# Performance work log

Hardware: AMD Instinct MI355X
Metric: run time of the kernel (lower is better)

Reference implementation:

```python
import jax, jax.numpy as jnp
import numpy as np

L, B, T, H = 4, 64, 256, 1024  # layers, batch, seq_len, hidden (=input=output size)


def setup_inputs() -> dict:
    key = jax.random.key(0)
    ks = jax.random.split(key, 5)
    s = 0.03  # ~1/sqrt(H) init scale to avoid gate saturation
    return {
        "x": jax.random.normal(ks[0], (B, T, H), dtype=jnp.float32),
        "W_ih": jax.random.normal(ks[1], (L, 4 * H, H), dtype=jnp.float32) * s,
        "W_hh": jax.random.normal(ks[2], (L, 4 * H, H), dtype=jnp.float32) * s,
        "b_ih": jax.random.normal(ks[3], (L, 4 * H), dtype=jnp.float32) * s,
        "b_hh": jax.random.normal(ks[4], (L, 4 * H), dtype=jnp.float32) * s,
    }


def _lstm_cell(xt, h, c, Wi, Wh, bi, bh):
    # PyTorch LSTMCell: gates = x W_ih^T + b_ih + h W_hh^T + b_hh; order i,f,g,o
    gates = xt @ Wi.T + bi + h @ Wh.T + bh  # [B, 4H]
    i, f, g, o = jnp.split(gates, 4, axis=-1)
    c_new = jax.nn.sigmoid(f) * c + jax.nn.sigmoid(i) * jnp.tanh(g)
    h_new = jax.nn.sigmoid(o) * jnp.tanh(c_new)
    return h_new, c_new


def reference(x, W_ih, W_hh, b_ih, b_hh):
    nlayers, bsz, hid = W_ih.shape[0], x.shape[0], W_hh.shape[-1]
    h0 = jnp.zeros((nlayers, bsz, hid), dtype=x.dtype)
    c0 = jnp.zeros((nlayers, bsz, hid), dtype=x.dtype)

    def step(carry, xt):  # xt: [B, H]
        h, c = carry  # [L, B, H] each
        inp = xt
        hs, cs = [], []
        for l in range(nlayers):  # small fixed layer loop
            h_l, c_l = _lstm_cell(inp, h[l], c[l], W_ih[l], W_hh[l], b_ih[l], b_hh[l])
            hs.append(h_l)
            cs.append(c_l)
            inp = h_l
        return (jnp.stack(hs), jnp.stack(cs)), None

    (h_fin, _), _ = jax.lax.scan(step, (h0, c0), jnp.swapaxes(x, 0, 1))
    return h_fin[-1]  # last layer's hidden at final timestep: [B, output_size]
```

## Files before the change

kernel.cpp:

```cpp
#include <hip/hip_runtime.h>

#define LAYERS 4
#define BATCH  64
#define SEQ    256
#define HID    1024

typedef _Float16 half8 __attribute__((ext_vector_type(8)));
typedef _Float16 half4 __attribute__((ext_vector_type(4)));
typedef float    f32x4 __attribute__((ext_vector_type(4)));
typedef unsigned long long u64;

__device__ __forceinline__ float sig_(float x) { return 1.0f / (1.0f + __expf(-x)); }
__device__ __forceinline__ float th_(float x)  { return 2.0f / (1.0f + __expf(-2.0f * x)) - 1.0f; }

__device__ __forceinline__ void llc_store_h4(_Float16* p, half4 v) {
    union { half4 h; u64 u; } cv; cv.h = v;
    __hip_atomic_store((u64*)p, cv.u, __ATOMIC_RELAXED, __HIP_MEMORY_SCOPE_AGENT);
}

struct BarSt {
    int arrive8[LAYERS][8][16];
    int rootL[LAYERS][16];
    int done8[LAYERS][8][16];
};

__global__ void k_bias(const float* __restrict__ bih, const float* __restrict__ bhh,
                       float* __restrict__ bias) {
    int i = blockIdx.x * blockDim.x + threadIdx.x;
    if (i < LAYERS * 4 * HID) bias[i] = bih[i] + bhh[i];
}

__global__ void k_packw(const float* __restrict__ wih32, const float* __restrict__ whh32,
                        _Float16* __restrict__ wpack) {
    unsigned c = blockIdx.x * blockDim.x + threadIdx.x;
    int lane = c & 63, g = (c >> 6) & 3, il = (c >> 8) & 7, q = (c >> 11) & 3;
    int jblk = (c >> 13) & 63, kh = (c >> 19) & 1, l = (int)(c >> 20);
    const float* src = (kh ? whh32 : wih32)
        + ((size_t)l * 4 * HID + (size_t)g * HID + jblk * 16 + (lane & 15)) * HID
        + (q * 8 + il) * 32 + (lane >> 4) * 8;
    f32x4 a = *(const f32x4*)src;
    f32x4 b = *(const f32x4*)(src + 4);
    half8 d;
    d[0]=(_Float16)a[0]; d[1]=(_Float16)a[1]; d[2]=(_Float16)a[2]; d[3]=(_Float16)a[3];
    d[4]=(_Float16)b[0]; d[5]=(_Float16)b[1]; d[6]=(_Float16)b[2]; d[7]=(_Float16)b[3];
    *(half8*)(wpack + (size_t)c * 8) = d;
}

__global__ void k_packx(const float* __restrict__ x32, _Float16* __restrict__ xpack) {
    unsigned c = blockIdx.x * blockDim.x + threadIdx.x;
    int lane = c & 63, i = (c >> 6) & 31, mt = (c >> 11) & 3, t = (int)(c >> 13);
    int m = mt * 16 + (lane & 15);
    int k = i * 32 + (lane >> 4) * 8;
    const float* src = x32 + ((size_t)m * SEQ + t) * HID + k;
    f32x4 a = *(const f32x4*)src;
    f32x4 b = *(const f32x4*)(src + 4);
    half8 d;
    d[0]=(_Float16)a[0]; d[1]=(_Float16)a[1]; d[2]=(_Float16)a[2]; d[3]=(_Float16)a[3];
    d[4]=(_Float16)b[0]; d[5]=(_Float16)b[1]; d[6]=(_Float16)b[2]; d[7]=(_Float16)b[3];
    *(half8*)(xpack + (size_t)c * 8) = d;
}

__global__ __launch_bounds__(512, 1) void k_persist(
        const _Float16* __restrict__ xpack,
        const _Float16* __restrict__ wpack,
        const float*    __restrict__ bih,
        const float*    __restrict__ bhh,
        _Float16*       __restrict__ hfull,
        BarSt*          __restrict__ bar,
        float*          __restrict__ out)
{
    const int layer = blockIdx.x >> 6;
    const int jblk  = blockIdx.x & 63;
    const int j0    = jblk << 4;
    const int oct   = jblk >> 3;
    const int tid   = threadIdx.x;
    const int wave  = tid >> 6;
    const int q     = wave & 3;
    const int kh    = wave >> 2;
    const int lane  = tid & 63;
    const int nl    = lane & 15;
    const int quad  = lane >> 4;
    const size_t BH = (size_t)BATCH * HID;

    __shared__ __align__(16) float gplane[2][4][4][32][20];
    __shared__ __align__(16) float cbuf[64][16];
    __shared__ __align__(16) float gbias[4][16];

    for (int i = tid; i < 64 * 16; i += 512) ((float*)cbuf)[i] = 0.0f;
    if (tid < 64) {
        int g = tid >> 4, col = tid & 15;
        size_t bidx = (size_t)layer * 4 * HID + (size_t)g * HID + j0 + col;
        gbias[g][col] = bih[bidx] + bhh[bidx];
    }

    const _Float16* Wp = wpack
        + ((((size_t)layer * 2 + kh) * 64 + jblk) * 4 + q) * 16384
        + (size_t)lane * 8;
    half8 wreg[8][4];
    #pragma unroll
    for (int il = 0; il < 8; ++il)
        #pragma unroll
        for (int g = 0; g < 4; ++g)
            wreg[il][g] = *(const half8*)(Wp + il * 2048 + g * 512);

    __syncthreads();

    const bool lastlayer = (layer == LAYERS - 1);

    for (int t = 0; t < SEQ; ++t) {
        if (lane == 0) {
            if (kh == 0) {
                if (layer > 0) {
                    while (__hip_atomic_load(&bar->done8[layer - 1][oct][0], __ATOMIC_RELAXED,
                                             __HIP_MEMORY_SCOPE_AGENT) < t + 1)
                        __builtin_amdgcn_s_sleep(1);
                }
            } else {
                if (t > 0) {
                    while (__hip_atomic_load(&bar->done8[layer][oct][0], __ATOMIC_RELAXED,
                                             __HIP_MEMORY_SCOPE_AGENT) < t)
                        __builtin_amdgcn_s_sleep(1);
                }
            }
        }
        __builtin_amdgcn_sched_barrier(0);
        asm volatile("" ::: "memory");

        const _Float16* Abase;
        if (kh == 0) {
            Abase = (layer == 0)
                ? (xpack + (size_t)t * BH)
                : (hfull + ((size_t)t * LAYERS + layer) * BH);
        } else {
            Abase = hfull + (t == 0 ? (size_t)0
                                    : ((size_t)(t - 1) * LAYERS + layer + 1)) * BH;
        }
        const _Float16* Ap = Abase + (size_t)q * 4096 + (size_t)lane * 8;

        f32x4 acc[4][4];
        #pragma unroll
        for (int mt = 0; mt < 4; ++mt)
            #pragma unroll
            for (int g = 0; g < 4; ++g) acc[mt][g] = (f32x4){0,0,0,0};

        #pragma unroll
        for (int il = 0; il < 8; ++il) {
            #pragma unroll
            for (int mt = 0; mt < 4; ++mt) {
                half8 a = *(const half8*)(Ap + (size_t)mt * 16384 + il * 512);
                acc[mt][0] = __builtin_amdgcn_mfma_f32_16x16x32_f16(a, wreg[il][0], acc[mt][0], 0,0,0);
                acc[mt][1] = __builtin_amdgcn_mfma_f32_16x16x32_f16(a, wreg[il][1], acc[mt][1], 0,0,0);
                acc[mt][2] = __builtin_amdgcn_mfma_f32_16x16x32_f16(a, wreg[il][2], acc[mt][2], 0,0,0);
                acc[mt][3] = __builtin_amdgcn_mfma_f32_16x16x32_f16(a, wreg[il][3], acc[mt][3], 0,0,0);
            }
        }

        _Float16* hp = hfull + ((size_t)t * LAYERS + layer + 1) * BH;
        const bool last = lastlayer && (t == SEQ - 1);

        if (kh == 1) {
            #pragma unroll
            for (int mt = 0; mt < 4; ++mt)
                #pragma unroll
                for (int g = 0; g < 4; ++g)
                    #pragma unroll
                    for (int r = 0; r < 4; ++r) {
                        int rm = mt * 16 + quad * 4 + r;
                        gplane[rm >> 5][q][g][rm & 31][nl] = acc[mt][g][r];
                    }
        }
        __syncthreads();
        if (kh == 0) {
            #pragma unroll
            for (int mt = 0; mt < 4; ++mt)
                #pragma unroll
                for (int g = 0; g < 4; ++g)
                    #pragma unroll
                    for (int r = 0; r < 4; ++r) {
                        int rm = mt * 16 + quad * 4 + r;
                        gplane[rm >> 5][q][g][rm & 31][nl] += acc[mt][g][r];
                    }
        }
        __syncthreads();
        if (tid < 256) {
            const int m  = tid >> 2;
            const int hb = m >> 5;
            const int ml = m & 31;
            const int jg = tid & 3;
            const int jA = j0 + jg * 4;

            f32x4 vi = *(const f32x4*)&gplane[hb][0][0][ml][jg*4] + *(const f32x4*)&gplane[hb][1][0][ml][jg*4]
                     + *(const f32x4*)&gplane[hb][2][0][ml][jg*4] + *(const f32x4*)&gplane[hb][3][0][ml][jg*4];
            f32x4 vf = *(const f32x4*)&gplane[hb][0][1][ml][jg*4] + *(const f32x4*)&gplane[hb][1][1][ml][jg*4]
                     + *(const f32x4*)&gplane[hb][2][1][ml][jg*4] + *(const f32x4*)&gplane[hb][3][1][ml][jg*4];
            f32x4 vg = *(const f32x4*)&gplane[hb][0][2][ml][jg*4] + *(const f32x4*)&gplane[hb][1][2][ml][jg*4]
                     + *(const f32x4*)&gplane[hb][2][2][ml][jg*4] + *(const f32x4*)&gplane[hb][3][2][ml][jg*4];
            f32x4 vo = *(const f32x4*)&gplane[hb][0][3][ml][jg*4] + *(const f32x4*)&gplane[hb][1][3][ml][jg*4]
                     + *(const f32x4*)&gplane[hb][2][3][ml][jg*4] + *(const f32x4*)&gplane[hb][3][3][ml][jg*4];

            f32x4 bi = *(const f32x4*)&gbias[0][jg*4];
            f32x4 bf = *(const f32x4*)&gbias[1][jg*4];
            f32x4 bg = *(const f32x4*)&gbias[2][jg*4];
            f32x4 bo = *(const f32x4*)&gbias[3][jg*4];

            f32x4 c = *(const f32x4*)&cbuf[m][jg*4];
            f32x4 cn, hn;
            #pragma unroll
            for (int i = 0; i < 4; ++i) {
                float gi = vi[i] + bi[i];
                float gf = vf[i] + bf[i];
                float gg = vg[i] + bg[i];
                float go = vo[i] + bo[i];
                cn[i] = sig_(gf) * c[i] + sig_(gi) * th_(gg);
                hn[i] = sig_(go) * th_(cn[i]);
            }
            *(f32x4*)&cbuf[m][jg*4] = cn;

            int i_ = jA >> 5, qd = (jA >> 3) & 3, jj = jA & 7;
            size_t hoff = (size_t)(m >> 4) * 16384 + (size_t)i_ * 512 + qd * 128 + (m & 15) * 8 + jj;
            half4 h4;
            h4[0]=(_Float16)hn[0]; h4[1]=(_Float16)hn[1]; h4[2]=(_Float16)hn[2]; h4[3]=(_Float16)hn[3];
            llc_store_h4(hp + hoff, h4);

            if (last) *(f32x4*)(out + (size_t)m * HID + jA) = hn;
        }

        asm volatile("s_waitcnt vmcnt(0)" ::: "memory");
        __syncthreads();
        if (tid == 0) {
            int a = __hip_atomic_fetch_add(&bar->arrive8[layer][oct][0], 1,
                        __ATOMIC_RELAXED, __HIP_MEMORY_SCOPE_AGENT) + 1;
            if (a == 8 * (t + 1)) {
                int r = __hip_atomic_fetch_add(&bar->rootL[layer][0], 1,
                            __ATOMIC_RELAXED, __HIP_MEMORY_SCOPE_AGENT) + 1;
                if (r == 8 * (t + 1)) {
                    #pragma unroll
                    for (int o = 0; o < 8; ++o)
                        __hip_atomic_store(&bar->done8[layer][o][0], t + 1,
                                __ATOMIC_RELAXED, __HIP_MEMORY_SCOPE_AGENT);
                }
            }
        }
    }
}

__global__ __launch_bounds__(512) void k_step(
        int s,
        const _Float16* __restrict__ xpack,
        const _Float16* __restrict__ wpack,
        const float*    __restrict__ bias,
        _Float16*       __restrict__ hbuf,
        float*          __restrict__ cst,
        float*          __restrict__ out)
{
    const int layer = blockIdx.x >> 6;
    const int t = s - layer;
    if (t < 0 || t >= SEQ) return;

    __shared__ __align__(16) float gplane[4][4][32][16];

    const int tid  = threadIdx.x;
    const int wave = tid >> 6;
    const int q    = wave & 3;
    const int kh   = wave >> 2;
    const int lane = tid & 63;
    const int nl   = lane & 15;
    const int quad = lane >> 4;
    const int jblk = blockIdx.x & 63;
    const int j0   = jblk << 4;
    const size_t BH = (size_t)BATCH * HID;

    const _Float16* Abase;
    if (kh == 0) {
        Abase = (layer == 0) ? (xpack + (size_t)t * BH)
                             : (hbuf + ((size_t)(layer - 1) * 2 + (t & 1)) * BH);
    } else {
        Abase = hbuf + ((size_t)layer * 2 + ((t + 1) & 1)) * BH;
    }
    const _Float16* Ap = Abase + (size_t)q * 4096 + (size_t)lane * 8;
    const _Float16* Wp = wpack
        + ((((size_t)layer * 2 + kh) * 64 + jblk) * 4 + q) * 16384
        + (size_t)lane * 8;

    f32x4 acc[4][4];
    #pragma unroll
    for (int mt = 0; mt < 4; ++mt)
        #pragma unroll
        for (int g = 0; g < 4; ++g) acc[mt][g] = (f32x4){0,0,0,0};

    #pragma unroll
    for (int il = 0; il < 8; ++il) {
        half8 w0 = *(const half8*)(Wp + il * 2048 + 0 * 512);
        half8 w1 = *(const half8*)(Wp + il * 2048 + 1 * 512);
        half8 w2 = *(const half8*)(Wp + il * 2048 + 2 * 512);
        half8 w3 = *(const half8*)(Wp + il * 2048 + 3 * 512);
        #pragma unroll
        for (int mt = 0; mt < 4; ++mt) {
            half8 a = *(const half8*)(Ap + (size_t)mt * 16384 + il * 512);
            acc[mt][0] = __builtin_amdgcn_mfma_f32_16x16x32_f16(a, w0, acc[mt][0], 0,0,0);
            acc[mt][1] = __builtin_amdgcn_mfma_f32_16x16x32_f16(a, w1, acc[mt][1], 0,0,0);
            acc[mt][2] = __builtin_amdgcn_mfma_f32_16x16x32_f16(a, w2, acc[mt][2], 0,0,0);
            acc[mt][3] = __builtin_amdgcn_mfma_f32_16x16x32_f16(a, w3, acc[mt][3], 0,0,0);
        }
    }

    const float* bb = bias + (size_t)layer * 4 * HID;
    _Float16* hp = hbuf + ((size_t)layer * 2 + (t & 1)) * BH;
    const bool last = (layer == LAYERS - 1) && (t == SEQ - 1);

    #pragma unroll
    for (int half = 0; half < 2; ++half) {
        if (kh == 1) {
            #pragma unroll
            for (int mtl = 0; mtl < 2; ++mtl)
                #pragma unroll
                for (int g = 0; g < 4; ++g)
                    #pragma unroll
                    for (int r = 0; r < 4; ++r)
                        gplane[q][g][mtl * 16 + quad * 4 + r][nl] = acc[half * 2 + mtl][g][r];
        }
        __syncthreads();
        if (kh == 0) {
            #pragma unroll
            for (int mtl = 0; mtl < 2; ++mtl)
                #pragma unroll
                for (int g = 0; g < 4; ++g)
                    #pragma unroll
                    for (int r = 0; r < 4; ++r)
                        gplane[q][g][mtl * 16 + quad * 4 + r][nl] += acc[half * 2 + mtl][g][r];
        }
        __syncthreads();
        if (tid < 128) {
            const int ml = tid >> 2;
            const int jg = tid & 3;
            const int m  = half * 32 + ml;
            const int jA = j0 + jg * 4;

            f32x4 vi = *(const f32x4*)&gplane[0][0][ml][jg*4] + *(const f32x4*)&gplane[1][0][ml][jg*4]
                     + *(const f32x4*)&gplane[2][0][ml][jg*4] + *(const f32x4*)&gplane[3][0][ml][jg*4];
            f32x4 vf = *(const f32x4*)&gplane[0][1][ml][jg*4] + *(const f32x4*)&gplane[1][1][ml][jg*4]
                     + *(const f32x4*)&gplane[2][1][ml][jg*4] + *(const f32x4*)&gplane[3][1][ml][jg*4];
            f32x4 vg = *(const f32x4*)&gplane[0][2][ml][jg*4] + *(const f32x4*)&gplane[1][2][ml][jg*4]
                     + *(const f32x4*)&gplane[2][2][ml][jg*4] + *(const f32x4*)&gplane[3][2][ml][jg*4];
            f32x4 vo = *(const f32x4*)&gplane[0][3][ml][jg*4] + *(const f32x4*)&gplane[1][3][ml][jg*4]
                     + *(const f32x4*)&gplane[2][3][ml][jg*4] + *(const f32x4*)&gplane[3][3][ml][jg*4];

            f32x4 bi = *(const f32x4*)(bb + 0 * HID + jA);
            f32x4 bf = *(const f32x4*)(bb + 1 * HID + jA);
            f32x4 bg = *(const f32x4*)(bb + 2 * HID + jA);
            f32x4 bo = *(const f32x4*)(bb + 3 * HID + jA);

            float* cp = cst + (size_t)layer * BH + (size_t)m * HID + jA;
            f32x4 c = *(const f32x4*)cp;
            f32x4 cn, hn;
            #pragma unroll
            for (int i = 0; i < 4; ++i) {
                float gi = vi[i] + bi[i];
                float gf = vf[i] + bf[i];
                float gg = vg[i] + bg[i];
                float go = vo[i] + bo[i];
                cn[i] = sig_(gf) * c[i] + sig_(gi) * th_(gg);
                hn[i] = sig_(go) * th_(cn[i]);
            }
            *(f32x4*)cp = cn;

            int i_ = jA >> 5, qd = (jA >> 3) & 3, jj = jA & 7;
            size_t hoff = (size_t)(m >> 4) * 16384 + (size_t)i_ * 512 + qd * 128 + (m & 15) * 8 + jj;
            half4 h4;
            h4[0]=(_Float16)hn[0]; h4[1]=(_Float16)hn[1]; h4[2]=(_Float16)hn[2]; h4[3]=(_Float16)hn[3];
            *(half4*)(hp + hoff) = h4;

            if (last) *(f32x4*)(out + (size_t)m * HID + jA) = hn;
        }
        __syncthreads();
    }
}

extern "C" void kernel_launch(void* const* d_in, const int* in_sizes, int n_in,
                              void* d_out, int out_size, void* d_ws, size_t ws_size,
                              hipStream_t stream) {
    const float* x32   = (const float*)d_in[0];
    const float* wih32 = (const float*)d_in[1];
    const float* whh32 = (const float*)d_in[2];
    const float* bih   = (const float*)d_in[3];
    const float* bhh   = (const float*)d_in[4];
    (void)in_sizes; (void)n_in; (void)out_size;

    const size_t BH = (size_t)BATCH * HID;
    char* ws = (char*)d_ws;
    size_t off = 0;
    _Float16* hpar  = (_Float16*)(ws + off); off += (size_t)LAYERS * 2 * BH * 2;
    float*    cst   = (float*)   (ws + off); off += (size_t)LAYERS * BH * 4;
    BarSt*    bar   = (BarSt*)   (ws + off); off += sizeof(BarSt);
    off = (off + 255) & ~(size_t)255;
    size_t zero_bytes = off;
    float*    bias  = (float*)   (ws + off); off += (size_t)LAYERS * 4 * HID * 4;
    _Float16* wpack = (_Float16*)(ws + off); off += (size_t)2 * LAYERS * 4 * HID * HID * 2;
    _Float16* xpack = (_Float16*)(ws + off); off += (size_t)SEQ * BH * 2;
    _Float16* hfull = (_Float16*)(ws + off);
    size_t full_need = off + (size_t)(SEQ * LAYERS + 1) * BH * 2;
    const int can_persist = (ws_size >= full_need) ? 1 : 0;

    hipMemsetAsync(ws, 0, zero_bytes, stream);
    if (can_persist) hipMemsetAsync(hfull, 0, BH * 2, stream);
    k_bias<<<(LAYERS * 4 * HID + 255) / 256, 256, 0, stream>>>(bih, bhh, bias);
    k_packw<<<(1u << 22) / 256, 256, 0, stream>>>(wih32, whh32, wpack);
    k_packx<<<(1u << 21) / 256, 256, 0, stream>>>(x32, xpack);

    hipError_t cerr = hipErrorUnknown;
    if (can_persist) {
        float* outp = (float*)d_out;
        _Float16* hfull_arg = hfull;
        void* kargs[] = { (void*)&xpack, (void*)&wpack, (void*)&bih, (void*)&bhh,
                          (void*)&hfull_arg, (void*)&bar, (void*)&outp };
        cerr = hipLaunchCooperativeKernel(
            k_persist, dim3(LAYERS * 64), dim3(512), kargs, 0u, stream);
    }

    if (cerr != hipSuccess) {
        for (int s = 0; s < SEQ + LAYERS - 1; ++s)
            k_step<<<LAYERS * 64, 512, 0, stream>>>(
                s, xpack, wpack, bias, hpar, cst, (float*)d_out);
    }
}
```

Before: 2.450 ms.

## Replace hierarchical done-flag barrier with direct polling of per-octet arrival counters

The two-level arrive/root/done barrier chain is removed. Each waiting wave now sums the eight per-octet arrival counters directly, which cuts the serialized atomic hops on the critical path between timesteps and layers. The kh==0 half now writes its partial gates to shared memory right after its own MFMAs, with the loop order changed so writes go out per m-tile. The pointwise LSTM cell work is spread over all 512 threads at two elements each instead of 256 threads at four. In exchange, every poll issues eight atomic loads instead of one, which adds traffic on those cache lines.

```diff
diff --git a/kernel.cpp b/kernel.cpp
--- a/kernel.cpp
+++ b/kernel.cpp
@@ -7,7 +7,9 @@
 
 typedef _Float16 half8 __attribute__((ext_vector_type(8)));
 typedef _Float16 half4 __attribute__((ext_vector_type(4)));
+typedef _Float16 half2v __attribute__((ext_vector_type(2)));
 typedef float    f32x4 __attribute__((ext_vector_type(4)));
+typedef float    f32x2 __attribute__((ext_vector_type(2)));
 typedef unsigned long long u64;
 
 __device__ __forceinline__ float sig_(float x) { return 1.0f / (1.0f + __expf(-x)); }
@@ -17,12 +19,26 @@
     union { half4 h; u64 u; } cv; cv.h = v;
     __hip_atomic_store((u64*)p, cv.u, __ATOMIC_RELAXED, __HIP_MEMORY_SCOPE_AGENT);
 }
+__device__ __forceinline__ void llc_store_h2(_Float16* p, half2v v) {
+    union { half2v h; unsigned u; } cv; cv.h = v;
+    __hip_atomic_store((unsigned*)p, cv.u, __ATOMIC_RELAXED, __HIP_MEMORY_SCOPE_AGENT);
+}
 
 struct BarSt {
     int arrive8[LAYERS][8][16];
-    int rootL[LAYERS][16];
-    int done8[LAYERS][8][16];
 };
+
+__device__ __forceinline__ void poll_sum8(const int (*lines)[16], int tgt) {
+    for (;;) {
+        int s = 0;
+        #pragma unroll
+        for (int o = 0; o < 8; ++o)
+            s += __hip_atomic_load(&lines[o][0], __ATOMIC_RELAXED,
+                                   __HIP_MEMORY_SCOPE_AGENT);
+        if (s >= tgt) return;
+        __builtin_amdgcn_s_sleep(1);
+    }
+}
 
 __global__ void k_bias(const float* __restrict__ bih, const float* __restrict__ bhh,
                        float* __restrict__ bias) {
@@ -108,59 +124,33 @@
     const bool lastlayer = (layer == LAYERS - 1);
 
     for (int t = 0; t < SEQ; ++t) {
-        if (lane == 0) {
-            if (kh == 0) {
-                if (layer > 0) {
-                    while (__hip_atomic_load(&bar->done8[layer - 1][oct][0], __ATOMIC_RELAXED,
-                                             __HIP_MEMORY_SCOPE_AGENT) < t + 1)
-                        __builtin_amdgcn_s_sleep(1);
-                }
-            } else {
-                if (t > 0) {
-                    while (__hip_atomic_load(&bar->done8[layer][oct][0], __ATOMIC_RELAXED,
-                                             __HIP_MEMORY_SCOPE_AGENT) < t)
-                        __builtin_amdgcn_s_sleep(1);
-                }
-            }
-        }
-        __builtin_amdgcn_sched_barrier(0);
-        asm volatile("" ::: "memory");
-
-        const _Float16* Abase;
-        if (kh == 0) {
-            Abase = (layer == 0)
-                ? (xpack + (size_t)t * BH)
-                : (hfull + ((size_t)t * LAYERS + layer) * BH);
-        } else {
-            Abase = hfull + (t == 0 ? (size_t)0
-                                    : ((size_t)(t - 1) * LAYERS + layer + 1)) * BH;
-        }
-        const _Float16* Ap = Abase + (size_t)q * 4096 + (size_t)lane * 8;
-
         f32x4 acc[4][4];
         #pragma unroll
         for (int mt = 0; mt < 4; ++mt)
             #pragma unroll
             for (int g = 0; g < 4; ++g) acc[mt][g] = (f32x4){0,0,0,0};
 
-        #pragma unroll
-        for (int il = 0; il < 8; ++il) {
+        if (kh == 0) {
+            if (lane == 0 && layer > 0)
+                poll_sum8(bar->arrive8[layer - 1], 64 * (t + 1));
+            __builtin_amdgcn_sched_barrier(0);
+            asm volatile("" ::: "memory");
+
+            const _Float16* Abase = (layer == 0)
+                ? (xpack + (size_t)t * BH)
+                : (hfull + ((size_t)t * LAYERS + layer) * BH);
+            const _Float16* Ap = Abase + (size_t)q * 4096 + (size_t)lane * 8;
+
             #pragma unroll
             for (int mt = 0; mt < 4; ++mt) {
-                half8 a = *(const half8*)(Ap + (size_t)mt * 16384 + il * 512);
-                acc[mt][0] = __builtin_amdgcn_mfma_f32_16x16x32_f16(a, wreg[il][0], acc[mt][0], 0,0,0);
-                acc[mt][1] = __builtin_amdgcn_mfma_f32_16x16x32_f16(a, wreg[il][1], acc[mt][1], 0,0,0);
-                acc[mt][2] = __builtin_amdgcn_mfma_f32_16x16x32_f16(a, wreg[il][2], acc[mt][2], 0,0,0);
-                acc[mt][3] = __builtin_amdgcn_mfma_f32_16x16x32_f16(a, wreg[il][3], acc[mt][3], 0,0,0);
-            }
-        }
-
-        _Float16* hp = hfull + ((size_t)t * LAYERS + layer + 1) * BH;
-        const bool last = lastlayer && (t == SEQ - 1);
-
-        if (kh == 1) {
-            #pragma unroll
-            for (int mt = 0; mt < 4; ++mt)
+                #pragma unroll
+                for (int il = 0; il < 8; ++il) {
+                    half8 a = *(const half8*)(Ap + (size_t)mt * 16384 + il * 512);
+                    acc[mt][0] = __builtin_amdgcn_mfma_f32_16x16x32_f16(a, wreg[il][0], acc[mt][0], 0,0,0);
+                    acc[mt][1] = __builtin_amdgcn_mfma_f32_16x16x32_f16(a, wreg[il][1], acc[mt][1], 0,0,0);
+                    acc[mt][2] = __builtin_amdgcn_mfma_f32_16x16x32_f16(a, wreg[il][2], acc[mt][2], 0,0,0);
+                    acc[mt][3] = __builtin_amdgcn_mfma_f32_16x16x32_f16(a, wreg[il][3], acc[mt][3], 0,0,0);
+                }
                 #pragma unroll
                 for (int g = 0; g < 4; ++g)
                     #pragma unroll
@@ -168,9 +158,33 @@
                         int rm = mt * 16 + quad * 4 + r;
                         gplane[rm >> 5][q][g][rm & 31][nl] = acc[mt][g][r];
                     }
-        }
-        __syncthreads();
-        if (kh == 0) {
+            }
+        } else {
+            if (lane == 0 && t > 0)
+                poll_sum8(bar->arrive8[layer], 64 * t);
+            __builtin_amdgcn_sched_barrier(0);
+            asm volatile("" ::: "memory");
+
+            const _Float16* Abase = hfull
+                + (t == 0 ? (size_t)0 : ((size_t)(t - 1) * LAYERS + layer + 1)) * BH;
+            const _Float16* Ap = Abase + (size_t)q * 4096 + (size_t)lane * 8;
+
+            #pragma unroll
+            for (int il = 0; il < 8; ++il) {
+                #pragma unroll
+                for (int mt = 0; mt < 4; ++mt) {
+                    half8 a = *(const half8*)(Ap + (size_t)mt * 16384 + il * 512);
+                    acc[mt][0] = __builtin_amdgcn_mfma_f32_16x16x32_f16(a, wreg[il][0], acc[mt][0], 0,0,0);
+                    acc[mt][1] = __builtin_amdgcn_mfma_f32_16x16x32_f16(a, wreg[il][1], acc[mt][1], 0,0,0);
+                    acc[mt][2] = __builtin_amdgcn_mfma_f32_16x16x32_f16(a, wreg[il][2], acc[mt][2], 0,0,0);
+                    acc[mt][3] = __builtin_amdgcn_mfma_f32_16x16x32_f16(a, wreg[il][3], acc[mt][3], 0,0,0);
+                }
+            }
+        }
+
+        __syncthreads();
+
+        if (kh == 1) {
             #pragma unroll
             for (int mt = 0; mt < 4; ++mt)
                 #pragma unroll
@@ -182,31 +196,34 @@
                     }
         }
         __syncthreads();
-        if (tid < 256) {
-            const int m  = tid >> 2;
+
+        _Float16* hp = hfull + ((size_t)t * LAYERS + layer + 1) * BH;
+        const bool last = lastlayer && (t == SEQ - 1);
+        {
+            const int m  = tid >> 3;
             const int hb = m >> 5;
             const int ml = m & 31;
-            const int jg = tid & 3;
-            const int jA = j0 + jg * 4;
-
-            f32x4 vi = *(const f32x4*)&gplane[hb][0][0][ml][jg*4] + *(const f32x4*)&gplane[hb][1][0][ml][jg*4]
-                     + *(const f32x4*)&gplane[hb][2][0][ml][jg*4] + *(const f32x4*)&gplane[hb][3][0][ml][jg*4];
-            f32x4 vf = *(const f32x4*)&gplane[hb][0][1][ml][jg*4] + *(const f32x4*)&gplane[hb][1][1][ml][jg*4]
-                     + *(const f32x4*)&gplane[hb][2][1][ml][jg*4] + *(const f32x4*)&gplane[hb][3][1][ml][jg*4];
-            f32x4 vg = *(const f32x4*)&gplane[hb][0][2][ml][jg*4] + *(const f32x4*)&gplane[hb][1][2][ml][jg*4]
-                     + *(const f32x4*)&gplane[hb][2][2][ml][jg*4] + *(const f32x4*)&gplane[hb][3][2][ml][jg*4];
-            f32x4 vo = *(const f32x4*)&gplane[hb][0][3][ml][jg*4] + *(const f32x4*)&gplane[hb][1][3][ml][jg*4]
-                     + *(const f32x4*)&gplane[hb][2][3][ml][jg*4] + *(const f32x4*)&gplane[hb][3][3][ml][jg*4];
-
-            f32x4 bi = *(const f32x4*)&gbias[0][jg*4];
-            f32x4 bf = *(const f32x4*)&gbias[1][jg*4];
-            f32x4 bg = *(const f32x4*)&gbias[2][jg*4];
-            f32x4 bo = *(const f32x4*)&gbias[3][jg*4];
-
-            f32x4 c = *(const f32x4*)&cbuf[m][jg*4];
-            f32x4 cn, hn;
-            #pragma unroll
-            for (int i = 0; i < 4; ++i) {
+            const int jg = tid & 7;
+            const int jA = j0 + jg * 2;
+
+            f32x2 vi = *(const f32x2*)&gplane[hb][0][0][ml][jg*2] + *(const f32x2*)&gplane[hb][1][0][ml][jg*2]
+                     + *(const f32x2*)&gplane[hb][2][0][ml][jg*2] + *(const f32x2*)&gplane[hb][3][0][ml][jg*2];
+            f32x2 vf = *(const f32x2*)&gplane[hb][0][1][ml][jg*2] + *(const f32x2*)&gplane[hb][1][1][ml][jg*2]
+                     + *(const f32x2*)&gplane[hb][2][1][ml][jg*2] + *(const f32x2*)&gplane[hb][3][1][ml][jg*2];
+            f32x2 vg = *(const f32x2*)&gplane[hb][0][2][ml][jg*2] + *(const f32x2*)&gplane[hb][1][2][ml][jg*2]
+                     + *(const f32x2*)&gplane[hb][2][2][ml][jg*2] + *(const f32x2*)&gplane[hb][3][2][ml][jg*2];
+            f32x2 vo = *(const f32x2*)&gplane[hb][0][3][ml][jg*2] + *(const f32x2*)&gplane[hb][1][3][ml][jg*2]
+                     + *(const f32x2*)&gplane[hb][2][3][ml][jg*2] + *(const f32x2*)&gplane[hb][3][3][ml][jg*2];
+
+            f32x2 bi = *(const f32x2*)&gbias[0][jg*2];
+            f32x2 bf = *(const f32x2*)&gbias[1][jg*2];
+            f32x2 bg = *(const f32x2*)&gbias[2][jg*2];
+            f32x2 bo = *(const f32x2*)&gbias[3][jg*2];
+
+            f32x2 c = *(const f32x2*)&cbuf[m][jg*2];
+            f32x2 cn, hn;
+            #pragma unroll
+            for (int i = 0; i < 2; ++i) {
                 float gi = vi[i] + bi[i];
                 float gf = vf[i] + bf[i];
                 float gg = vg[i] + bg[i];
@@ -214,33 +231,22 @@
                 cn[i] = sig_(gf) * c[i] + sig_(gi) * th_(gg);
                 hn[i] = sig_(go) * th_(cn[i]);
             }
-            *(f32x4*)&cbuf[m][jg*4] = cn;
+            *(f32x2*)&cbuf[m][jg*2] = cn;
 
             int i_ = jA >> 5, qd = (jA >> 3) & 3, jj = jA & 7;
             size_t hoff = (size_t)(m >> 4) * 16384 + (size_t)i_ * 512 + qd * 128 + (m & 15) * 8 + jj;
-            half4 h4;
-            h4[0]=(_Float16)hn[0]; h4[1]=(_Float16)hn[1]; h4[2]=(_Float16)hn[2]; h4[3]=(_Float16)hn[3];
-            llc_store_h4(hp + hoff, h4);
-
-            if (last) *(f32x4*)(out + (size_t)m * HID + jA) = hn;
+            half2v h2;
+            h2[0] = (_Float16)hn[0]; h2[1] = (_Float16)hn[1];
+            llc_store_h2(hp + hoff, h2);
+
+            if (last) *(f32x2*)(out + (size_t)m * HID + jA) = hn;
         }
 
         asm volatile("s_waitcnt vmcnt(0)" ::: "memory");
         __syncthreads();
-        if (tid == 0) {
-            int a = __hip_atomic_fetch_add(&bar->arrive8[layer][oct][0], 1,
-                        __ATOMIC_RELAXED, __HIP_MEMORY_SCOPE_AGENT) + 1;
-            if (a == 8 * (t + 1)) {
-                int r = __hip_atomic_fetch_add(&bar->rootL[layer][0], 1,
-                            __ATOMIC_RELAXED, __HIP_MEMORY_SCOPE_AGENT) + 1;
-                if (r == 8 * (t + 1)) {
-                    #pragma unroll
-                    for (int o = 0; o < 8; ++o)
-                        __hip_atomic_store(&bar->done8[layer][o][0], t + 1,
-                                __ATOMIC_RELAXED, __HIP_MEMORY_SCOPE_AGENT);
-                }
-            }
-        }
+        if (tid == 0)
+            __hip_atomic_fetch_add(&bar->arrive8[layer][oct][0], 1,
+                                   __ATOMIC_RELAXED, __HIP_MEMORY_SCOPE_AGENT);
     }
 }
 
```

Measured after the change: 2.581 ms. 1.05x slower.

## Replace hierarchical atomic barrier with per-block flags polled by whole wave

Applied to the files above, without the earlier changes.

Replaces the two-level arrive/root counter barrier with one flag per block per layer. Each block stores its timestep once done, and waiting waves have all 64 lanes load the 64 flags of a layer and use __all to check completion. This removes the serialized fetch_add chain and the extra hop through the root counter before release, which shortens the critical path of each recurrent step. In exchange, every waiting wave polls 64 flags instead of one, which adds memory traffic while spinning. Flags are packed contiguously, so many blocks contend on the same cache lines.

```diff
diff --git a/kernel.cpp b/kernel.cpp
--- a/kernel.cpp
+++ b/kernel.cpp
@@ -19,9 +19,7 @@
 }
 
 struct BarSt {
-    int arrive8[LAYERS][8][16];
-    int rootL[LAYERS][16];
-    int done8[LAYERS][8][16];
+    int flag[LAYERS][64];
 };
 
 __global__ void k_bias(const float* __restrict__ bih, const float* __restrict__ bhh,
@@ -72,7 +70,6 @@
     const int layer = blockIdx.x >> 6;
     const int jblk  = blockIdx.x & 63;
     const int j0    = jblk << 4;
-    const int oct   = jblk >> 3;
     const int tid   = threadIdx.x;
     const int wave  = tid >> 6;
     const int q     = wave & 3;
@@ -108,18 +105,24 @@
     const bool lastlayer = (layer == LAYERS - 1);
 
     for (int t = 0; t < SEQ; ++t) {
-        if (lane == 0) {
-            if (kh == 0) {
-                if (layer > 0) {
-                    while (__hip_atomic_load(&bar->done8[layer - 1][oct][0], __ATOMIC_RELAXED,
-                                             __HIP_MEMORY_SCOPE_AGENT) < t + 1)
-                        __builtin_amdgcn_s_sleep(1);
+        if (kh == 0) {
+            if (layer > 0) {
+                const int tgt = t + 1;
+                for (;;) {
+                    int v = __hip_atomic_load(&bar->flag[layer - 1][lane],
+                                              __ATOMIC_RELAXED, __HIP_MEMORY_SCOPE_AGENT);
+                    if (__all(v >= tgt)) break;
+                    __builtin_amdgcn_s_sleep(1);
                 }
-            } else {
-                if (t > 0) {
-                    while (__hip_atomic_load(&bar->done8[layer][oct][0], __ATOMIC_RELAXED,
-                                             __HIP_MEMORY_SCOPE_AGENT) < t)
-                        __builtin_amdgcn_s_sleep(1);
+            }
+        } else {
+            if (t > 0) {
+                const int tgt = t;
+                for (;;) {
+                    int v = __hip_atomic_load(&bar->flag[layer][lane],
+                                              __ATOMIC_RELAXED, __HIP_MEMORY_SCOPE_AGENT);
+                    if (__all(v >= tgt)) break;
+                    __builtin_amdgcn_s_sleep(1);
                 }
             }
         }
@@ -227,20 +230,9 @@
 
         asm volatile("s_waitcnt vmcnt(0)" ::: "memory");
         __syncthreads();
-        if (tid == 0) {
-            int a = __hip_atomic_fetch_add(&bar->arrive8[layer][oct][0], 1,
-                        __ATOMIC_RELAXED, __HIP_MEMORY_SCOPE_AGENT) + 1;
-            if (a == 8 * (t + 1)) {
-                int r = __hip_atomic_fetch_add(&bar->rootL[layer][0], 1,
-                            __ATOMIC_RELAXED, __HIP_MEMORY_SCOPE_AGENT) + 1;
-                if (r == 8 * (t + 1)) {
-                    #pragma unroll
-                    for (int o = 0; o < 8; ++o)
-                        __hip_atomic_store(&bar->done8[layer][o][0], t + 1,
-                                __ATOMIC_RELAXED, __HIP_MEMORY_SCOPE_AGENT);
-                }
-            }
-        }
+        if (tid == 0)
+            __hip_atomic_store(&bar->flag[layer][jblk], t + 1,
+                               __ATOMIC_RELAXED, __HIP_MEMORY_SCOPE_AGENT);
     }
 }
 
```

Result: slower. 2.853 ms (+16.5%).
